# Optimization experiments

Measured on AMD Instinct MI355X. Metric: run time of the kernel, lower is better.

## Reference

```python
import jax, jax.numpy as jnp
import numpy as np
from jax import lax

N, E, B, HW, CIN, HID = 50000, 800000, 32, 128, 8, 128


def conv2d(x, w, b):
    # NCHW, OIHW, SAME padding, stride 1
    y = lax.conv_general_dilated(x, w, (1, 1), 'SAME',
                                 dimension_numbers=('NCHW', 'OIHW', 'NCHW'))
    return y + b[None, :, None, None]


def setup_inputs() -> dict:
    key = jax.random.key(0)
    ks = jax.random.split(key, 24)
    inp = {}
    inp['xdata128'] = jax.random.normal(ks[0], (B, CIN, HW, HW), jnp.float32)
    inp['x'] = jax.random.normal(ks[1], (N, 8), jnp.float32)
    inp['pos'] = jax.random.uniform(ks[2], (N, 2), jnp.float32) * 20.0
    inp['edge_index'] = jax.random.randint(ks[3], (2, E), 0, N, jnp.int32)
    inp['batch'] = jnp.sort(jax.random.randint(ks[4], (N,), 0, B, jnp.int32))
    # CNN stand-in for Modfiedunet4shrink: 8->16->16->1, 3x3 SAME
    s = 0.1
    inp['w1'] = jax.random.normal(ks[5], (16, CIN, 3, 3), jnp.float32) * s
    inp['b1'] = jnp.zeros((16,), jnp.float32)
    inp['w2'] = jax.random.normal(ks[6], (16, 16, 3, 3), jnp.float32) * s
    inp['b2'] = jnp.zeros((16,), jnp.float32)
    inp['w3'] = jax.random.normal(ks[7], (1, 16, 3, 3), jnp.float32) * s
    inp['b3'] = jnp.zeros((1,), jnp.float32)
    # GraphSAGE: 4 SAGEConv layers (mean aggr): 8->128->128->128->1
    dims = [(HID, 8), (HID, HID), (HID, HID), (1, HID)]
    for i, (o, iC) in enumerate(dims, start=1):
        sc = 1.0 / np.sqrt(iC)
        inp[f'Wl{i}'] = jax.random.normal(ks[8 + 2 * i], (o, iC), jnp.float32) * sc
        inp[f'Wr{i}'] = jax.random.normal(ks[9 + 2 * i], (o, iC), jnp.float32) * sc
        inp[f'bs{i}'] = jnp.zeros((o,), jnp.float32)
    return inp


def _sage_conv(h, edge_index, Wl, Wr, b):
    src, dst = edge_index[0], edge_index[1]
    deg = jax.ops.segment_sum(jnp.ones((E,), h.dtype), dst, num_segments=N)
    agg = jax.ops.segment_sum(h[src], dst, num_segments=N)
    agg = agg / jnp.clip(deg, 1.0)[:, None]          # mean aggregation
    return agg @ Wl.T + h @ Wr.T + b


def reference(xdata128, x, pos, edge_index, batch,
              w1, b1, w2, b2, w3, b3,
              Wl1, Wr1, bs1, Wl2, Wr2, bs2, Wl3, Wr3, bs3, Wl4, Wr4, bs4):
    # --- CNN (Modfiedunet4shrink stand-in), keeps 128x128, 1 output channel ---
    h = jax.nn.relu(conv2d(xdata128, w1, b1))
    h = jax.nn.relu(conv2d(h, w2, b2))
    x1 = conv2d(h, w3, b3)                            # [B, 1, 128, 128]

    # --- cnntogra: gather CNN features at per-node pixel locations ---
    # selected_images[inverse_indices] == datatomap[batch]
    pidx = jnp.round(pos / 20.0 * (HW - 1)).astype(jnp.int32)
    pidx = jnp.clip(pidx, 0, HW - 1)
    r, c = pidx[:, 1], pidx[:, 0]                     # (row=y-index, col=x-index)
    cnng = x1[batch, :, r, c]                         # [N, 1]

    # --- graph features: cat(x[:,0:2], x[:,-3:], pos, cnng) -> [N, 8] ---
    gx = jnp.concatenate([x[:, 0:2], x[:, -3:], pos, cnng], axis=-1)

    # --- GraphSAGE, 4 layers, ReLU between, no act on last ---
    h = jax.nn.relu(_sage_conv(gx, edge_index, Wl1, Wr1, bs1))
    h = jax.nn.relu(_sage_conv(h, edge_index, Wl2, Wr2, bs2))
    h = jax.nn.relu(_sage_conv(h, edge_index, Wl3, Wr3, bs3))
    gout = _sage_conv(h, edge_index, Wl4, Wr4, bs4)   # [N, 1]
    return (x1, gout)
```

## Files before the change

### kernel.cpp

```cpp
#include <hip/hip_runtime.h>

#define N_NODES 50000
#define N_EDGES 800000
#define NBATCH 32
#define HWDIM 128
#define IMG (HWDIM * HWDIM)
#define HID 128
#define NBKT ((N_NODES + 255) / 256)
#define NB 625
#define EPB 1280
#define LDSP 40

typedef float f32x4 __attribute__((ext_vector_type(4)));
typedef __bf16 bf16x8 __attribute__((ext_vector_type(8)));
typedef unsigned short u16x8 __attribute__((ext_vector_type(8)));

__device__ __forceinline__ unsigned short f2bf(float x) {
  unsigned u = __builtin_bit_cast(unsigned, x);
  u = (u + 0x7FFF + ((u >> 16) & 1)) >> 16;
  return (unsigned short)u;
}
__device__ __forceinline__ float bf2f(unsigned short h) {
  return __builtin_bit_cast(float, (unsigned)h << 16);
}

__global__ __launch_bounds__(256) void prep_kernel(
    const int* __restrict__ ei, int* __restrict__ cnt_mat,
    const float* __restrict__ Wl2, const float* __restrict__ Wr2,
    const float* __restrict__ Wl3, const float* __restrict__ Wr3,
    const float* __restrict__ w1, const float* __restrict__ w2,
    unsigned short* __restrict__ Wb2, unsigned short* __restrict__ Wb3,
    unsigned short* __restrict__ Wc1, unsigned short* __restrict__ Wc2) {
  __shared__ int hist[NBKT];
  int t = threadIdx.x;
  if (blockIdx.x < NB) {
    if (t < NBKT) hist[t] = 0;
    __syncthreads();
    int e0 = blockIdx.x * EPB;
#pragma unroll
    for (int i = 0; i < EPB / 256; ++i) {
      int d = ei[N_EDGES + e0 + i * 256 + t];
      atomicAdd(&hist[d >> 8], 1);
    }
    __syncthreads();
    if (t < NBKT) cnt_mat[t * NB + blockIdx.x] = hist[t];
    return;
  }
  int tt = (blockIdx.x - NB) * 256 + t;
  if (tt < 65536) {
    const float* Wl = (tt < 32768) ? Wl2 : Wl3;
    const float* Wr = (tt < 32768) ? Wr2 : Wr3;
    unsigned short* Wb = (tt < 32768) ? Wb2 : Wb3;
    int q = tt & 32767;
    int j = q >> 8, k = q & 255;
    float v = (k < 128) ? Wl[j * 128 + k] : Wr[j * 128 + (k - 128)];
    Wb[q] = f2bf(v);
    return;
  }
  int t2 = tt - 65536;
  const float* w;
  unsigned short* dst;
  int CIN, idx;
  if (t2 < 1536) {
    w = w1; dst = Wc1; CIN = 8; idx = t2;
  } else if (t2 < 1536 + 2560) {
    w = w2; dst = Wc2; CIN = 16; idx = t2 - 1536;
  } else {
    return;
  }
  int j = idx & 7;
  int n = (idx >> 3) & 15;
  int sgi = idx >> 7;
  int k = sgi * 8 + j;
  int tap = k / CIN;
  int ci = k % CIN;
  dst[idx] = (tap < 9) ? f2bf(w[(n * CIN + ci) * 9 + tap]) : (unsigned short)0;
}

__global__ __launch_bounds__(256) void conv1_mfma_kernel(
    const float* __restrict__ in, const unsigned short* __restrict__ Wc,
    const float* __restrict__ bias, unsigned short* __restrict__ out) {
  __shared__ unsigned short lds[10 * 130 * 8];
  int tid = threadIdx.x;
  int img = blockIdx.x >> 4;
  int y0 = (blockIdx.x & 15) * 8;
  int lane = tid & 63, wave = tid >> 6;
  int l15 = lane & 15, g = lane >> 4;

  const float* sb = in + (size_t)img * 8 * IMG;
#pragma unroll
  for (int i = 0; i < 5; ++i) {
    int idx = tid + i * 256;
    int r = idx >> 7;
    int x = idx & 127;
    int gy = y0 - 1 + r;
    u16x8 v = {};
    if ((unsigned)gy < (unsigned)HWDIM) {
      const float* sp = sb + gy * HWDIM + x;
#pragma unroll
      for (int ci = 0; ci < 8; ++ci) v[ci] = f2bf(sp[ci * IMG]);
    }
    *(u16x8*)&lds[(r * 130 + x + 1) * 8] = v;
  }
  if (tid < 20) {
    int r = tid >> 1, c = (tid & 1) * 129;
    *(u16x8*)&lds[(r * 130 + c) * 8] = (u16x8){};
  }

  bf16x8 bfrag[3];
  int adel[3];
#pragma unroll
  for (int s = 0; s < 3; ++s) {
    bfrag[s] = __builtin_bit_cast(bf16x8, *(const u16x8*)(Wc + (((s * 4 + g) * 16) + l15) * 8));
    int tap = (32 * s + 8 * g) / 8;
    tap = tap > 8 ? 8 : tap;
    adel[s] = ((tap / 3) * 130 + (tap % 3)) * 8;
  }
  float bv = bias[l15];
  __syncthreads();

#pragma unroll
  for (int ti = 0; ti < 16; ++ti) {
    int tile = wave * 16 + ti;
    int ly = tile >> 3, xb = (tile & 7) * 16;
    int tb = (ly * 130 + xb + l15) * 8;
    f32x4 acc = {};
#pragma unroll
    for (int s = 0; s < 3; ++s) {
      bf16x8 a = __builtin_bit_cast(bf16x8, *(const u16x8*)&lds[tb + adel[s]]);
      acc = __builtin_amdgcn_mfma_f32_16x16x32_bf16(a, bfrag[s], acc, 0, 0, 0);
    }
    size_t base = (((size_t)img * HWDIM + y0 + ly) * HWDIM + xb);
#pragma unroll
    for (int r = 0; r < 4; ++r) {
      float v = fmaxf(acc[r] + bv, 0.0f);
      out[(base + g * 4 + r) * 16 + l15] = f2bf(v);
    }
  }
}

__global__ __launch_bounds__(256) void conv2_mfma_kernel(
    const unsigned short* __restrict__ in, const unsigned short* __restrict__ Wc,
    const float* __restrict__ bias, unsigned short* __restrict__ out) {
  __shared__ unsigned short lds[10 * 130 * 24];
  int tid = threadIdx.x;
  int img = blockIdx.x >> 4;
  int y0 = (blockIdx.x & 15) * 8;
  int lane = tid & 63, wave = tid >> 6;
  int l15 = lane & 15, g = lane >> 4;

  const unsigned short* sb = in + (size_t)img * IMG * 16;
#pragma unroll
  for (int i = 0; i < 10; ++i) {
    int idx = tid + i * 256;
    int r = idx >> 8;
    int x = (idx & 255) >> 1;
    int hh = idx & 1;
    int gy = y0 - 1 + r;
    u16x8 v = {};
    if ((unsigned)gy < (unsigned)HWDIM) v = *(const u16x8*)(sb + ((size_t)gy * HWDIM + x) * 16 + hh * 8);
    *(u16x8*)&lds[(r * 130 + x + 1) * 24 + hh * 8] = v;
  }
  if (tid < 20) {
    int r = tid >> 1, c = (tid & 1) * 129;
#pragma unroll
    for (int q = 0; q < 3; ++q) *(u16x8*)&lds[(r * 130 + c) * 24 + q * 8] = (u16x8){};
  }

  bf16x8 bfrag[5];
  int adel[5];
#pragma unroll
  for (int s = 0; s < 5; ++s) {
    bfrag[s] = __builtin_bit_cast(bf16x8, *(const u16x8*)(Wc + (((s * 4 + g) * 16) + l15) * 8));
    int tap = (32 * s + 8 * g) / 16;
    tap = tap > 8 ? 8 : tap;
    adel[s] = ((tap / 3) * 130 + (tap % 3)) * 24 + (g & 1) * 8;
  }
  float bv = bias[l15];
  __syncthreads();

#pragma unroll
  for (int ti = 0; ti < 16; ++ti) {
    int tile = wave * 16 + ti;
    int ly = tile >> 3, xb = (tile & 7) * 16;
    int tb = (ly * 130 + xb + l15) * 24;
    f32x4 acc = {};
#pragma unroll
    for (int s = 0; s < 5; ++s) {
      bf16x8 a = __builtin_bit_cast(bf16x8, *(const u16x8*)&lds[tb + adel[s]]);
      acc = __builtin_amdgcn_mfma_f32_16x16x32_bf16(a, bfrag[s], acc, 0, 0, 0);
    }
    size_t base = (((size_t)img * HWDIM + y0 + ly) * HWDIM + xb);
#pragma unroll
    for (int r = 0; r < 4; ++r) {
      float v = fmaxf(acc[r] + bv, 0.0f);
      out[(base + g * 4 + r) * 16 + l15] = f2bf(v);
    }
  }
}

__global__ __launch_bounds__(256) void conv3_f32_kernel(const unsigned short* __restrict__ h2,
                                                        const float* __restrict__ w3,
                                                        const float* __restrict__ b3,
                                                        float* __restrict__ x1) {
  __shared__ float w9[9][16];
  __shared__ float b3s;
  int tid = threadIdx.x;
  if (tid < 144) {
    int ci = tid & 15, tap = tid >> 4;
    w9[tap][ci] = w3[ci * 9 + tap];
  }
  if (tid == 144) b3s = b3[0];
  __syncthreads();
  int t = blockIdx.x * 256 + tid;
  int x = t & 127;
  int y = (t >> 7) & 127;
  int img = t >> 14;
  float acc = b3s;
#pragma unroll
  for (int dy = 0; dy < 3; ++dy) {
    int yy = y + dy - 1;
    if ((unsigned)yy >= (unsigned)HWDIM) continue;
#pragma unroll
    for (int dx = 0; dx < 3; ++dx) {
      int xx = x + dx - 1;
      if ((unsigned)xx >= (unsigned)HWDIM) continue;
      const u16x8* p = (const u16x8*)(h2 + (((size_t)img * HWDIM + yy) * HWDIM + xx) * 16);
      u16x8 lo = p[0], hi = p[1];
      const float* wt = w9[dy * 3 + dx];
#pragma unroll
      for (int j = 0; j < 8; ++j) acc += bf2f(lo[j]) * wt[j];
#pragma unroll
      for (int j = 0; j < 8; ++j) acc += bf2f(hi[j]) * wt[8 + j];
    }
  }
  x1[(size_t)img * IMG + y * HWDIM + x] = acc;
}

__global__ __launch_bounds__(1024) void scan_rows_kernel(const int* __restrict__ cnt_mat,
                                                         int* __restrict__ rowscan,
                                                         int* __restrict__ row_total) {
  __shared__ int wsum[16];
  int row = blockIdx.x;
  int t = threadIdx.x;
  int lane = t & 63, w = t >> 6;
  int v = (t < NB) ? cnt_mat[row * NB + t] : 0;
  int s = v;
#pragma unroll
  for (int off = 1; off < 64; off <<= 1) {
    int u = __shfl_up(s, off, 64);
    if (lane >= off) s += u;
  }
  if (lane == 63) wsum[w] = s;
  __syncthreads();
  if (w == 0 && lane < 16) {
    int ws = wsum[lane];
#pragma unroll
    for (int off = 1; off < 16; off <<= 1) {
      int u = __shfl_up(ws, off, 64);
      if (lane >= off) ws += u;
    }
    wsum[lane] = ws;
  }
  __syncthreads();
  int base = (w > 0) ? wsum[w - 1] : 0;
  int incl = s + base;
  if (t < NB) rowscan[row * NB + t] = incl - v;
  if (t == NB - 1) row_total[row] = incl;
}

__device__ __forceinline__ void scan_bases(const int* __restrict__ row_total, int* bb,
                                           int* wsum) {
  int t = threadIdx.x;
  int lane = t & 63, w = t >> 6;
  int v = (t < NBKT) ? row_total[t] : 0;
  int s = v;
#pragma unroll
  for (int off = 1; off < 64; off <<= 1) {
    int u = __shfl_up(s, off, 64);
    if (lane >= off) s += u;
  }
  if (lane == 63) wsum[w] = s;
  __syncthreads();
  int add = 0;
#pragma unroll
  for (int i = 0; i < 4; ++i)
    if (i < w) add += wsum[i];
  if (t < NBKT) bb[t] = s + add - v;
  __syncthreads();
}

__global__ __launch_bounds__(256) void scatter2_kernel(const int* __restrict__ ei,
                                                       const int* __restrict__ rowscan,
                                                       const int* __restrict__ row_total,
                                                       int* __restrict__ bucket_data) {
  __shared__ int bb[NBKT];
  __shared__ int lhist[NBKT];
  __shared__ int lexcl[NBKT];
  __shared__ int gb[NBKT];
  __shared__ int wsum[4];
  __shared__ int lds_pack[EPB];
  __shared__ int lds_dest[EPB];
  int t = threadIdx.x;
  int blk = blockIdx.x;
  scan_bases(row_total, bb, wsum);
  if (t < NBKT) lhist[t] = 0;
  __syncthreads();
  int e0 = blk * EPB;
  int myb[EPB / 256], myp[EPB / 256], mypack[EPB / 256];
#pragma unroll
  for (int i = 0; i < EPB / 256; ++i) {
    int e = e0 + i * 256 + t;
    int s = ei[e];
    int d = ei[N_EDGES + e];
    int b = d >> 8;
    myb[i] = b;
    mypack[i] = s | ((d & 255) << 16);
    myp[i] = atomicAdd(&lhist[b], 1);
  }
  __syncthreads();
  {
    int lane = t & 63, w = t >> 6;
    int v = (t < NBKT) ? lhist[t] : 0;
    int s = v;
#pragma unroll
    for (int off = 1; off < 64; off <<= 1) {
      int u = __shfl_up(s, off, 64);
      if (lane >= off) s += u;
    }
    if (lane == 63) wsum[w] = s;
    __syncthreads();
    int add = 0;
#pragma unroll
    for (int i = 0; i < 4; ++i)
      if (i < w) add += wsum[i];
    if (t < NBKT) {
      lexcl[t] = s + add - v;
      gb[t] = bb[t] + rowscan[t * NB + blk];
    }
  }
  __syncthreads();
#pragma unroll
  for (int i = 0; i < EPB / 256; ++i) {
    int slot = lexcl[myb[i]] + myp[i];
    lds_pack[slot] = mypack[i];
    lds_dest[slot] = gb[myb[i]] + myp[i];
  }
  __syncthreads();
#pragma unroll
  for (int i = 0; i < EPB / 256; ++i) {
    int slot = i * 256 + t;
    bucket_data[lds_dest[slot]] = lds_pack[slot];
  }
}

__global__ __launch_bounds__(256) void bucketB_kernel(
    const int* __restrict__ row_total, const int* __restrict__ bucket_data,
    int* __restrict__ row_ptr, int* __restrict__ csr,
    const float* __restrict__ x, const float* __restrict__ pos,
    const int* __restrict__ batch, const float* __restrict__ x1,
    float* __restrict__ gx) {
  __shared__ int bb[NBKT];
  __shared__ int cnts[256];
  __shared__ int curs[256];
  __shared__ int wsum[4];
  int b = blockIdx.x;
  int t = threadIdx.x;
  {
    int i = b * 256 + t;
    if (i < N_NODES) {
      float px = pos[2 * i + 0];
      float py = pos[2 * i + 1];
      int cx = (int)rintf(px / 20.0f * 127.0f);
      int cy = (int)rintf(py / 20.0f * 127.0f);
      cx = min(max(cx, 0), HWDIM - 1);
      cy = min(max(cy, 0), HWDIM - 1);
      int bi = batch[i];
      float cn = x1[(size_t)bi * IMG + cy * HWDIM + cx];
      const float* xr = x + (size_t)i * 8;
      float* g = gx + (size_t)i * 8;
      g[0] = xr[0];
      g[1] = xr[1];
      g[2] = xr[5];
      g[3] = xr[6];
      g[4] = xr[7];
      g[5] = px;
      g[6] = py;
      g[7] = cn;
    }
  }
  scan_bases(row_total, bb, wsum);
  int cnt = row_total[b];
  int base = bb[b];
  if (b == 0 && t == 0) row_ptr[N_NODES] = N_EDGES;
  cnts[t] = 0;
  __syncthreads();
  const int* bd = bucket_data + base;
  for (int k = t; k < cnt; k += 256) {
    int v = bd[k];
    atomicAdd(&cnts[(v >> 16) & 255], 1);
  }
  __syncthreads();
  int v = cnts[t];
  int lane = t & 63, w = t >> 6;
  int s = v;
#pragma unroll
  for (int off = 1; off < 64; off <<= 1) {
    int u = __shfl_up(s, off, 64);
    if (lane >= off) s += u;
  }
  if (lane == 63) wsum[w] = s;
  __syncthreads();
  int add = 0;
#pragma unroll
  for (int i = 0; i < 4; ++i)
    if (i < w) add += wsum[i];
  int excl = s + add - v;
  int node = b * 256 + t;
  if (node < N_NODES) row_ptr[node] = base + excl;
  curs[t] = excl;
  __syncthreads();
  for (int k = t; k < cnt; k += 256) {
    int vv = bd[k];
    int p = atomicAdd(&curs[(vv >> 16) & 255], 1);
    csr[base + p] = vv & 0xffff;
  }
}

__global__ __launch_bounds__(256) void l1_fused_kernel(
    const float* __restrict__ gx, const int* __restrict__ row_ptr,
    const int* __restrict__ csr, const float* __restrict__ Wl,
    const float* __restrict__ Wr, const float* __restrict__ b,
    unsigned short* __restrict__ out) {
  __shared__ float wl[8][128];
  __shared__ float wr[8][128];
  __shared__ float aggs[32][8];
  int tid = threadIdx.x;
  for (int t = tid; t < 1024; t += 256) {
    int j = t >> 3, k = t & 7;
    wl[k][j] = Wl[t];
    wr[k][j] = Wr[t];
  }
  int node0 = blockIdx.x * 32;
  {
    int i = node0 + (tid >> 3);
    int f = tid & 7;
    float acc = 0.0f;
    if (i < N_NODES) {
      int beg = row_ptr[i], end = row_ptr[i + 1];
      int k = beg;
      for (; k + 2 <= end; k += 2) {
        int s0 = csr[k], s1 = csr[k + 1];
        acc += gx[(size_t)s0 * 8 + f] + gx[(size_t)s1 * 8 + f];
      }
      for (; k < end; ++k) acc += gx[(size_t)csr[k] * 8 + f];
      acc /= fmaxf((float)(end - beg), 1.0f);
    }
    aggs[tid >> 3][f] = acc;
  }
  __syncthreads();
  int nl = tid >> 3;
  int i = node0 + nl;
  if (i >= N_NODES) return;
  float av[8], gv[8];
#pragma unroll
  for (int k = 0; k < 8; ++k) {
    av[k] = aggs[nl][k];
    gv[k] = gx[(size_t)i * 8 + k];
  }
  int c0 = (tid & 7) * 16;
#pragma unroll
  for (int c = 0; c < 16; ++c) {
    int col = c0 + c;
    float acc = b[col];
#pragma unroll
    for (int k = 0; k < 8; ++k) acc += av[k] * wl[k][col] + gv[k] * wr[k][col];
    out[(size_t)i * HID + col] = f2bf(fmaxf(acc, 0.0f));
  }
}

__global__ __launch_bounds__(256) void agg128_bf16_kernel(
    const unsigned short* __restrict__ h, const int* __restrict__ row_ptr,
    const int* __restrict__ csr, unsigned short* __restrict__ out) {
  int wid = (blockIdx.x * blockDim.x + threadIdx.x) >> 6;
  int lane = threadIdx.x & 63;
  if (wid >= N_NODES) return;
  int beg = __builtin_amdgcn_readfirstlane(row_ptr[wid]);
  int end = __builtin_amdgcn_readfirstlane(row_ptr[wid + 1]);
  float ax = 0.0f, ay = 0.0f;
  const unsigned short* hp = h + 2 * lane;
  int k = beg;
  for (; k + 4 <= end; k += 4) {
    int s0 = csr[k];
    int s1 = csr[k + 1];
    int s2 = csr[k + 2];
    int s3 = csr[k + 3];
    unsigned v0 = *(const unsigned*)(hp + (size_t)s0 * HID);
    unsigned v1 = *(const unsigned*)(hp + (size_t)s1 * HID);
    unsigned v2 = *(const unsigned*)(hp + (size_t)s2 * HID);
    unsigned v3 = *(const unsigned*)(hp + (size_t)s3 * HID);
    ax += (bf2f(v0 & 0xffff) + bf2f(v1 & 0xffff)) + (bf2f(v2 & 0xffff) + bf2f(v3 & 0xffff));
    ay += (bf2f(v0 >> 16) + bf2f(v1 >> 16)) + (bf2f(v2 >> 16) + bf2f(v3 >> 16));
  }
  for (; k < end; ++k) {
    int s = csr[k];
    unsigned v = *(const unsigned*)(hp + (size_t)s * HID);
    ax += bf2f(v & 0xffff);
    ay += bf2f(v >> 16);
  }
  float inv = 1.0f / fmaxf((float)(end - beg), 1.0f);
  unsigned o = (unsigned)f2bf(ax * inv) | ((unsigned)f2bf(ay * inv) << 16);
  *(unsigned*)(out + (size_t)wid * HID + 2 * lane) = o;
}

__global__ __launch_bounds__(256) void sage_gemm_mfma_kernel(
    const unsigned short* __restrict__ A1, const unsigned short* __restrict__ A2,
    const unsigned short* __restrict__ Wb, const float* __restrict__ bias,
    unsigned short* __restrict__ C, int M, int do_relu,
    const float* __restrict__ Wl4, const float* __restrict__ Wr4,
    float* __restrict__ z, float* __restrict__ zr, int do_zzr) {
  __shared__ unsigned short Alds[64 * LDSP];
  __shared__ unsigned short Wlds[128 * LDSP];
  int tid = threadIdx.x;
  int wave = tid >> 6, lane = tid & 63;
  int l15 = lane & 15, g = lane >> 4;
  int row0 = blockIdx.x * 64;

  f32x4 acc[8];
#pragma unroll
  for (int n = 0; n < 8; ++n) acc[n] = (f32x4){0.f, 0.f, 0.f, 0.f};

  for (int ks = 0; ks < 8; ++ks) {
    const unsigned short* Asrc = (ks < 4) ? A1 : A2;
    int k0 = (ks & 3) * 32;
    {
      int r = tid >> 2, cc = tid & 3;
      int gr = row0 + r;
      u16x8 v = {};
      if (gr < M) v = *(const u16x8*)(Asrc + (size_t)gr * HID + k0 + cc * 8);
      *(u16x8*)(&Alds[r * LDSP + cc * 8]) = v;
    }
#pragma unroll
    for (int it = 0; it < 2; ++it) {
      int c = tid + it * 256;
      int j = c >> 2, cc = c & 3;
      u16x8 wv = *(const u16x8*)(Wb + j * 256 + ks * 32 + cc * 8);
      *(u16x8*)(&Wlds[j * LDSP + cc * 8]) = wv;
    }
    __syncthreads();

    bf16x8 a = __builtin_bit_cast(bf16x8, *(const u16x8*)(&Alds[(wave * 16 + l15) * LDSP + g * 8]));
#pragma unroll
    for (int n = 0; n < 8; ++n) {
      bf16x8 w = __builtin_bit_cast(bf16x8, *(const u16x8*)(&Wlds[(16 * n + l15) * LDSP + g * 8]));
      acc[n] = __builtin_amdgcn_mfma_f32_16x16x32_bf16(a, w, acc[n], 0, 0, 0);
    }
    __syncthreads();
  }

  float wl4v[8], wr4v[8];
  if (do_zzr) {
#pragma unroll
    for (int n = 0; n < 8; ++n) {
      wl4v[n] = Wl4[16 * n + l15];
      wr4v[n] = Wr4[16 * n + l15];
    }
  }
  float zp[4] = {0.f, 0.f, 0.f, 0.f};
  float zrp[4] = {0.f, 0.f, 0.f, 0.f};

#pragma unroll
  for (int n = 0; n < 8; ++n) {
    int col = 16 * n + l15;
    float bv = bias[col];
#pragma unroll
    for (int r = 0; r < 4; ++r) {
      int grow = row0 + wave * 16 + g * 4 + r;
      float v = acc[n][r] + bv;
      if (do_relu) v = fmaxf(v, 0.0f);
      if (grow < M) C[(size_t)grow * HID + col] = f2bf(v);
      if (do_zzr) {
        zp[r] += v * wl4v[n];
        zrp[r] += v * wr4v[n];
      }
    }
  }
  if (do_zzr) {
#pragma unroll
    for (int r = 0; r < 4; ++r) {
      float a = zp[r], c = zrp[r];
#pragma unroll
      for (int off = 1; off < 16; off <<= 1) {
        a += __shfl_xor(a, off, 64);
        c += __shfl_xor(c, off, 64);
      }
      int grow = row0 + wave * 16 + g * 4 + r;
      if (l15 == 0 && grow < M) {
        z[grow] = a;
        zr[grow] = c;
      }
    }
  }
}

__global__ void gout_kernel(const float* __restrict__ z, const float* __restrict__ zr,
                            const int* __restrict__ row_ptr, const int* __restrict__ csr,
                            const float* __restrict__ bs4, float* __restrict__ gout) {
  int i = blockIdx.x * blockDim.x + threadIdx.x;
  if (i >= N_NODES) return;
  int beg = row_ptr[i], end = row_ptr[i + 1];
  float s = 0.0f;
  int k = beg;
  for (; k + 2 <= end; k += 2) s += z[csr[k]] + z[csr[k + 1]];
  for (; k < end; ++k) s += z[csr[k]];
  float d = fmaxf((float)(end - beg), 1.0f);
  gout[i] = s / d + zr[i] + bs4[0];
}

extern "C" void kernel_launch(void* const* d_in, const int* in_sizes, int n_in,
                              void* d_out, int out_size, void* d_ws, size_t ws_size,
                              hipStream_t stream) {
  const float* xdata = (const float*)d_in[0];
  const float* x = (const float*)d_in[1];
  const float* pos = (const float*)d_in[2];
  const int* ei = (const int*)d_in[3];
  const int* batch = (const int*)d_in[4];
  const float* w1 = (const float*)d_in[5];
  const float* b1 = (const float*)d_in[6];
  const float* w2 = (const float*)d_in[7];
  const float* b2 = (const float*)d_in[8];
  const float* w3 = (const float*)d_in[9];
  const float* b3 = (const float*)d_in[10];
  const float* Wl1 = (const float*)d_in[11];
  const float* Wr1 = (const float*)d_in[12];
  const float* bs1 = (const float*)d_in[13];
  const float* Wl2 = (const float*)d_in[14];
  const float* Wr2 = (const float*)d_in[15];
  const float* bs2 = (const float*)d_in[16];
  const float* Wl3 = (const float*)d_in[17];
  const float* Wr3 = (const float*)d_in[18];
  const float* bs3 = (const float*)d_in[19];
  const float* Wl4 = (const float*)d_in[20];
  const float* Wr4 = (const float*)d_in[21];
  const float* bs4 = (const float*)d_in[22];

  float* x1_out = (float*)d_out;
  float* gout = (float*)d_out + (size_t)NBATCH * IMG;

  char* ws = (char*)d_ws;
  size_t off = 0;
  auto take = [&](size_t bytes) -> char* {
    char* p = ws + off;
    off = (off + bytes + 255) & ~(size_t)255;
    return p;
  };
  float* hbuf1 = (float*)take((size_t)NBATCH * 16 * IMG * 4);
  float* hbuf2 = (float*)take((size_t)NBATCH * 16 * IMG * 4);
  unsigned short* aggb = (unsigned short*)take((size_t)N_NODES * HID * 2);
  float* gx = (float*)take((size_t)N_NODES * 8 * 4);
  int* row_ptr = (int*)take((size_t)(N_NODES + 1) * 4);
  int* csr = (int*)take((size_t)N_EDGES * 4);
  int* cnt_mat = (int*)take((size_t)NBKT * NB * 4);
  int* rowscan = (int*)take((size_t)NBKT * NB * 4);
  int* row_total = (int*)take((size_t)NBKT * 4);
  int* bucket_data = (int*)take((size_t)N_EDGES * 4);
  float* z = (float*)take((size_t)N_NODES * 4);
  float* zr = (float*)take((size_t)N_NODES * 4);
  unsigned short* Wb2 = (unsigned short*)take((size_t)128 * 256 * 2);
  unsigned short* Wb3 = (unsigned short*)take((size_t)128 * 256 * 2);
  unsigned short* Wc1 = (unsigned short*)take((size_t)12 * 128 * 2);
  unsigned short* Wc2 = (unsigned short*)take((size_t)20 * 128 * 2);
  (void)ws_size;

  unsigned short* h1c = (unsigned short*)hbuf1;
  unsigned short* h2c = (unsigned short*)hbuf2;
  unsigned short* h1 = (unsigned short*)hbuf1;
  unsigned short* h2 = (unsigned short*)hbuf2;
  unsigned short* h3 = (unsigned short*)hbuf1;

  const int nblk_n = (N_NODES + 255) / 256;
  const int nblk_conv = NBATCH * 16;
  const int nblk_gemm = (N_NODES + 63) / 64;

  hipLaunchKernelGGL(prep_kernel, dim3(NB + 273), dim3(256), 0, stream, ei, cnt_mat, Wl2, Wr2,
                     Wl3, Wr3, w1, w2, Wb2, Wb3, Wc1, Wc2);

  hipLaunchKernelGGL(conv1_mfma_kernel, dim3(nblk_conv), dim3(256), 0, stream, xdata, Wc1, b1,
                     h1c);
  hipLaunchKernelGGL(conv2_mfma_kernel, dim3(nblk_conv), dim3(256), 0, stream, h1c, Wc2, b2,
                     h2c);
  hipLaunchKernelGGL(conv3_f32_kernel, dim3(NBATCH * IMG / 256), dim3(256), 0, stream, h2c, w3,
                     b3, x1_out);

  hipLaunchKernelGGL(scan_rows_kernel, dim3(NBKT), dim3(1024), 0, stream, cnt_mat, rowscan,
                     row_total);
  hipLaunchKernelGGL(scatter2_kernel, dim3(NB), dim3(256), 0, stream, ei, rowscan, row_total,
                     bucket_data);
  hipLaunchKernelGGL(bucketB_kernel, dim3(NBKT), dim3(256), 0, stream, row_total, bucket_data,
                     row_ptr, csr, x, pos, batch, x1_out, gx);

  hipLaunchKernelGGL(l1_fused_kernel, dim3((N_NODES + 31) / 32), dim3(256), 0, stream, gx,
                     row_ptr, csr, Wl1, Wr1, bs1, h1);

  hipLaunchKernelGGL(agg128_bf16_kernel, dim3(N_NODES / 4), dim3(256), 0, stream, h1, row_ptr,
                     csr, aggb);
  hipLaunchKernelGGL(sage_gemm_mfma_kernel, dim3(nblk_gemm), dim3(256), 0, stream, aggb, h1,
                     Wb2, bs2, h2, N_NODES, 1, (const float*)nullptr, (const float*)nullptr,
                     (float*)nullptr, (float*)nullptr, 0);

  hipLaunchKernelGGL(agg128_bf16_kernel, dim3(N_NODES / 4), dim3(256), 0, stream, h2, row_ptr,
                     csr, aggb);
  hipLaunchKernelGGL(sage_gemm_mfma_kernel, dim3(nblk_gemm), dim3(256), 0, stream, aggb, h2,
                     Wb3, bs3, h3, N_NODES, 1, Wl4, Wr4, z, zr, 1);

  hipLaunchKernelGGL(gout_kernel, dim3(nblk_n), dim3(256), 0, stream, z, zr, row_ptr, csr, bs4,
                     gout);
}
```

Measured before the change: 180.0 us.

## Fuse neighbor mean aggregation into SAGE MFMA GEMM via LDS staging

Merges the separate gather-mean aggregation kernel into the SAGE GEMM kernel. Each block aggregates its 64 nodes' neighbor features into a padded LDS tile, then feeds that tile directly as the first half of the K dimension to the MFMA loop. This removes the global round trip of the aggregated bf16 buffer and one launch per layer. The cost is lower parallelism for the latency-bound gather: each wave now walks 16 nodes serially, and there are far fewer blocks, with more LDS per block that may reduce occupancy.

```diff
diff --git a/kernel.cpp b/kernel.cpp
--- a/kernel.cpp
+++ b/kernel.cpp
@@ -10,6 +10,7 @@
 #define NB 625
 #define EPB 1280
 #define LDSP 40
+#define AGGP 136
 
 typedef float f32x4 __attribute__((ext_vector_type(4)));
 typedef __bf16 bf16x8 __attribute__((ext_vector_type(8)));
@@ -479,46 +480,13 @@
   }
 }
 
-__global__ __launch_bounds__(256) void agg128_bf16_kernel(
+__global__ __launch_bounds__(256) void sage_layer_kernel(
     const unsigned short* __restrict__ h, const int* __restrict__ row_ptr,
-    const int* __restrict__ csr, unsigned short* __restrict__ out) {
-  int wid = (blockIdx.x * blockDim.x + threadIdx.x) >> 6;
-  int lane = threadIdx.x & 63;
-  if (wid >= N_NODES) return;
-  int beg = __builtin_amdgcn_readfirstlane(row_ptr[wid]);
-  int end = __builtin_amdgcn_readfirstlane(row_ptr[wid + 1]);
-  float ax = 0.0f, ay = 0.0f;
-  const unsigned short* hp = h + 2 * lane;
-  int k = beg;
-  for (; k + 4 <= end; k += 4) {
-    int s0 = csr[k];
-    int s1 = csr[k + 1];
-    int s2 = csr[k + 2];
-    int s3 = csr[k + 3];
-    unsigned v0 = *(const unsigned*)(hp + (size_t)s0 * HID);
-    unsigned v1 = *(const unsigned*)(hp + (size_t)s1 * HID);
-    unsigned v2 = *(const unsigned*)(hp + (size_t)s2 * HID);
-    unsigned v3 = *(const unsigned*)(hp + (size_t)s3 * HID);
-    ax += (bf2f(v0 & 0xffff) + bf2f(v1 & 0xffff)) + (bf2f(v2 & 0xffff) + bf2f(v3 & 0xffff));
-    ay += (bf2f(v0 >> 16) + bf2f(v1 >> 16)) + (bf2f(v2 >> 16) + bf2f(v3 >> 16));
-  }
-  for (; k < end; ++k) {
-    int s = csr[k];
-    unsigned v = *(const unsigned*)(hp + (size_t)s * HID);
-    ax += bf2f(v & 0xffff);
-    ay += bf2f(v >> 16);
-  }
-  float inv = 1.0f / fmaxf((float)(end - beg), 1.0f);
-  unsigned o = (unsigned)f2bf(ax * inv) | ((unsigned)f2bf(ay * inv) << 16);
-  *(unsigned*)(out + (size_t)wid * HID + 2 * lane) = o;
-}
-
-__global__ __launch_bounds__(256) void sage_gemm_mfma_kernel(
-    const unsigned short* __restrict__ A1, const unsigned short* __restrict__ A2,
-    const unsigned short* __restrict__ Wb, const float* __restrict__ bias,
-    unsigned short* __restrict__ C, int M, int do_relu,
+    const int* __restrict__ csr, const unsigned short* __restrict__ Wb,
+    const float* __restrict__ bias, unsigned short* __restrict__ C, int M, int do_relu,
     const float* __restrict__ Wl4, const float* __restrict__ Wr4,
     float* __restrict__ z, float* __restrict__ zr, int do_zzr) {
+  __shared__ unsigned short Agg[64 * AGGP];
   __shared__ unsigned short Alds[64 * LDSP];
   __shared__ unsigned short Wlds[128 * LDSP];
   int tid = threadIdx.x;
@@ -526,18 +494,51 @@
   int l15 = lane & 15, g = lane >> 4;
   int row0 = blockIdx.x * 64;
 
+  const unsigned short* hp = h + 2 * lane;
+  for (int ii = 0; ii < 16; ++ii) {
+    int r = wave * 16 + ii;
+    int i = row0 + r;
+    float ax = 0.f, ay = 0.f, inv = 0.f;
+    if (i < M) {
+      int beg = __builtin_amdgcn_readfirstlane(row_ptr[i]);
+      int end = __builtin_amdgcn_readfirstlane(row_ptr[i + 1]);
+      int k = beg;
+      for (; k + 4 <= end; k += 4) {
+        int s0 = csr[k];
+        int s1 = csr[k + 1];
+        int s2 = csr[k + 2];
+        int s3 = csr[k + 3];
+        unsigned v0 = *(const unsigned*)(hp + (size_t)s0 * HID);
+        unsigned v1 = *(const unsigned*)(hp + (size_t)s1 * HID);
+        unsigned v2 = *(const unsigned*)(hp + (size_t)s2 * HID);
+        unsigned v3 = *(const unsigned*)(hp + (size_t)s3 * HID);
+        ax += (bf2f(v0 & 0xffff) + bf2f(v1 & 0xffff)) + (bf2f(v2 & 0xffff) + bf2f(v3 & 0xffff));
+        ay += (bf2f(v0 >> 16) + bf2f(v1 >> 16)) + (bf2f(v2 >> 16) + bf2f(v3 >> 16));
+      }
+      for (; k < end; ++k) {
+        int s = csr[k];
+        unsigned v = *(const unsigned*)(hp + (size_t)s * HID);
+        ax += bf2f(v & 0xffff);
+        ay += bf2f(v >> 16);
+      }
+      inv = 1.0f / fmaxf((float)(end - beg), 1.0f);
+    }
+    unsigned o = (unsigned)f2bf(ax * inv) | ((unsigned)f2bf(ay * inv) << 16);
+    *(unsigned*)&Agg[r * AGGP + 2 * lane] = o;
+  }
+  __syncthreads();
+
   f32x4 acc[8];
 #pragma unroll
   for (int n = 0; n < 8; ++n) acc[n] = (f32x4){0.f, 0.f, 0.f, 0.f};
 
   for (int ks = 0; ks < 8; ++ks) {
-    const unsigned short* Asrc = (ks < 4) ? A1 : A2;
     int k0 = (ks & 3) * 32;
-    {
+    if (ks >= 4) {
       int r = tid >> 2, cc = tid & 3;
       int gr = row0 + r;
       u16x8 v = {};
-      if (gr < M) v = *(const u16x8*)(Asrc + (size_t)gr * HID + k0 + cc * 8);
+      if (gr < M) v = *(const u16x8*)(h + (size_t)gr * HID + k0 + cc * 8);
       *(u16x8*)(&Alds[r * LDSP + cc * 8]) = v;
     }
 #pragma unroll
@@ -549,7 +550,13 @@
     }
     __syncthreads();
 
-    bf16x8 a = __builtin_bit_cast(bf16x8, *(const u16x8*)(&Alds[(wave * 16 + l15) * LDSP + g * 8]));
+    bf16x8 a;
+    if (ks < 4)
+      a = __builtin_bit_cast(bf16x8,
+          *(const u16x8*)(&Agg[(wave * 16 + l15) * AGGP + ks * 32 + g * 8]));
+    else
+      a = __builtin_bit_cast(bf16x8,
+          *(const u16x8*)(&Alds[(wave * 16 + l15) * LDSP + g * 8]));
 #pragma unroll
     for (int n = 0; n < 8; ++n) {
       bf16x8 w = __builtin_bit_cast(bf16x8, *(const u16x8*)(&Wlds[(16 * n + l15) * LDSP + g * 8]));
@@ -656,7 +663,6 @@
   };
   float* hbuf1 = (float*)take((size_t)NBATCH * 16 * IMG * 4);
   float* hbuf2 = (float*)take((size_t)NBATCH * 16 * IMG * 4);
-  unsigned short* aggb = (unsigned short*)take((size_t)N_NODES * HID * 2);
   float* gx = (float*)take((size_t)N_NODES * 8 * 4);
   int* row_ptr = (int*)take((size_t)(N_NODES + 1) * 4);
   int* csr = (int*)take((size_t)N_EDGES * 4);
@@ -702,16 +708,12 @@
   hipLaunchKernelGGL(l1_fused_kernel, dim3((N_NODES + 31) / 32), dim3(256), 0, stream, gx,
                      row_ptr, csr, Wl1, Wr1, bs1, h1);
 
-  hipLaunchKernelGGL(agg128_bf16_kernel, dim3(N_NODES / 4), dim3(256), 0, stream, h1, row_ptr,
-                     csr, aggb);
-  hipLaunchKernelGGL(sage_gemm_mfma_kernel, dim3(nblk_gemm), dim3(256), 0, stream, aggb, h1,
-                     Wb2, bs2, h2, N_NODES, 1, (const float*)nullptr, (const float*)nullptr,
-                     (float*)nullptr, (float*)nullptr, 0);
-
-  hipLaunchKernelGGL(agg128_bf16_kernel, dim3(N_NODES / 4), dim3(256), 0, stream, h2, row_ptr,
-                     csr, aggb);
-  hipLaunchKernelGGL(sage_gemm_mfma_kernel, dim3(nblk_gemm), dim3(256), 0, stream, aggb, h2,
-                     Wb3, bs3, h3, N_NODES, 1, Wl4, Wr4, z, zr, 1);
+  hipLaunchKernelGGL(sage_layer_kernel, dim3(nblk_gemm), dim3(256), 0, stream, h1, row_ptr,
+                     csr, Wb2, bs2, h2, N_NODES, 1, (const float*)nullptr,
+                     (const float*)nullptr, (float*)nullptr, (float*)nullptr, 0);
+
+  hipLaunchKernelGGL(sage_layer_kernel, dim3(nblk_gemm), dim3(256), 0, stream, h2, row_ptr,
+                     csr, Wb3, bs3, h3, N_NODES, 1, Wl4, Wr4, z, zr, 1);
 
   hipLaunchKernelGGL(gout_kernel, dim3(nblk_n), dim3(256), 0, stream, z, zr, row_ptr, csr, bs4,
                      gout);
```

After: 204.1 us. 1.13x slower.
